# Performance work log

Measured on AMD Instinct MI355X. Metric: run time of the kernel, lower is better.

The kernel has to match this reference:

```python
import jax, jax.numpy as jnp
import numpy as np

B, S, D, H = 2, 2048, 1024, 16
DH = D // H  # key_dim = embed_dim // num_heads
NEG = 1e9    # Keras masked-softmax adder magnitude
EPS = 1e-6


def setup_inputs() -> dict:
    key = jax.random.key(0)
    ks = jax.random.split(key, 6)
    sc = 1.0 / np.sqrt(D)
    return {
        "x": jax.random.normal(ks[0], (B, S, D), jnp.float32),
        "Wq": jax.random.normal(ks[1], (D, H, DH), jnp.float32) * sc,
        "bq": jnp.zeros((H, DH), jnp.float32),
        "Wk": jax.random.normal(ks[2], (D, H, DH), jnp.float32) * sc,
        "bk": jnp.zeros((H, DH), jnp.float32),
        "Wv": jax.random.normal(ks[3], (D, H, DH), jnp.float32) * sc,
        "bv": jnp.zeros((H, DH), jnp.float32),
        "Wo": jax.random.normal(ks[4], (H, DH, D), jnp.float32) * (1.0 / np.sqrt(D)),
        "bo": jnp.zeros((D,), jnp.float32),
        "gamma": jnp.ones((D,), jnp.float32),
        "beta": jnp.zeros((D,), jnp.float32),
    }


def reference(x, Wq, bq, Wk, bk, Wv, bv, Wo, bo, gamma, beta):
    # Keras MultiHeadAttention(query=x, value=x), inference (dropouts are identity)
    q = jnp.einsum("bsd,dhk->bshk", x, Wq) + bq  # [B,S,H,DH]
    k = jnp.einsum("bsd,dhk->bshk", x, Wk) + bk
    v = jnp.einsum("bsd,dhk->bshk", x, Wv) + bv

    scores = jnp.einsum("bqhd,bkhd->bhqk", q, k) / jnp.sqrt(jnp.asarray(DH, x.dtype))
    # Source: mask = 1 - band_part(ones, -1, 0) -> ones strictly ABOVE diagonal.
    # Keras attends where mask==1 and adds (1-mask)*(-1e9) elsewhere. Faithful:
    i = jnp.arange(S)[:, None]
    j = jnp.arange(S)[None, :]
    allowed = (j > i).astype(scores.dtype)  # [S,S], strict upper triangle
    scores = scores + (allowed - 1.0) * NEG  # subtract 1e9 where not allowed
    probs = jax.nn.softmax(scores, axis=-1)

    ctx = jnp.einsum("bhqk,bkhd->bqhd", probs, v)  # [B,S,H,DH]
    attn_out = jnp.einsum("bqhd,hdo->bqo", ctx, Wo) + bo  # [B,S,D]

    # residual + LayerNorm(eps=1e-6)
    y = x + attn_out
    mu = jnp.mean(y, axis=-1, keepdims=True)
    var = jnp.mean(jnp.square(y - mu), axis=-1, keepdims=True)
    return (y - mu) * jax.lax.rsqrt(var + EPS) * gamma + beta
```

## Files before the change

### kernel.cpp

```cpp
#include <hip/hip_runtime.h>
#include <hip/hip_bf16.h>

typedef __hip_bfloat16 bf16;
typedef __attribute__((ext_vector_type(8))) short bf16x8;
typedef __attribute__((ext_vector_type(4))) float f32x4;

constexpr int Bc  = 2;
constexpr int Sc  = 2048;
constexpr int Dc  = 1024;
constexpr int Hc  = 16;
constexpr int DHc = 64;
constexpr int BS  = Bc * Sc;
constexpr int NT  = Sc / 64;

__device__ __forceinline__ float bs2f(unsigned short u) {
    union { unsigned int i; float f; } v; v.i = ((unsigned int)u) << 16; return v.f;
}
__device__ __forceinline__ short f2bs(float x) {
    bf16 h = __float2bfloat16(x);
    return *reinterpret_cast<short*>(&h);
}

typedef const __attribute__((address_space(1))) unsigned int* as1_u32p;
typedef __attribute__((address_space(3))) unsigned int* as3_u32p;
__device__ __forceinline__ void gl_lds16(const void* g, void* l) {
    __builtin_amdgcn_global_load_lds((as1_u32p)g, (as3_u32p)l, 16, 0, 0);
}

__global__ __launch_bounds__(256) void cast_x(const float* __restrict__ in,
                                              short* __restrict__ out) {
    const int i = (blockIdx.x * 256 + threadIdx.x) * 4;
    const float4 v = *(const float4*)(in + i);
    ushort4 o;
    o.x = (unsigned short)f2bs(v.x);
    o.y = (unsigned short)f2bs(v.y);
    o.z = (unsigned short)f2bs(v.z);
    o.w = (unsigned short)f2bs(v.w);
    *(ushort4*)(out + i) = o;
}

__global__ __launch_bounds__(256) void transpose_cast(
    const float* __restrict__ w0, const float* __restrict__ w1,
    const float* __restrict__ w2, const float* __restrict__ w3,
    short* __restrict__ outbase)
{
    __shared__ float T[64][65];
    const int z = blockIdx.z;
    const float* in = (z == 0) ? w0 : (z == 1) ? w1 : (z == 2) ? w2 : w3;
    short* out = outbase + (size_t)z * 1024 * 1024;
    const int k0 = blockIdx.x * 64, n0 = blockIdx.y * 64;
    const int t = threadIdx.x;
    #pragma unroll
    for (int it = 0; it < 4; ++it) {
        const int s = it * 256 + t;
        const int r = s >> 4, c = (s & 15) * 4;
        *(float4*)&T[r][c] = *(const float4*)(in + (size_t)(k0 + r) * 1024 + n0 + c);
    }
    __syncthreads();
    #pragma unroll
    for (int it = 0; it < 4; ++it) {
        const int s = it * 256 + t;
        const int rr = s >> 4, cc = (s & 15) * 4;
        ushort4 o;
        o.x = (unsigned short)f2bs(T[cc + 0][rr]);
        o.y = (unsigned short)f2bs(T[cc + 1][rr]);
        o.z = (unsigned short)f2bs(T[cc + 2][rr]);
        o.w = (unsigned short)f2bs(T[cc + 3][rr]);
        *(ushort4*)(out + (size_t)(n0 + rr) * 1024 + k0 + cc) = o;
    }
}

__global__ __launch_bounds__(256, 3) void gemm_bt(
    const short* __restrict__ A, const short* __restrict__ BTbase,
    const float* __restrict__ b0, const float* __restrict__ b1,
    const float* __restrict__ b2, short* __restrict__ Cbase,
    const float sc0)
{
    __shared__ __align__(16) short As[128 * 64];
    __shared__ __align__(16) short Bs[128 * 64];

    const int z = blockIdx.z;
    const short* BT = BTbase + (size_t)z * 1024 * 1024;
    const float* bias = (z == 0) ? b0 : (z == 1) ? b1 : b2;
    const float sc = (z == 0) ? sc0 : 1.0f;
    short* C = Cbase + (size_t)z * BS * Dc;

    const int t = threadIdx.x;
    const int lane = t & 63, w = t >> 6;
    const int quad = lane >> 4, l16 = lane & 15;
    const int wm = (w & 1) * 64, wn = (w >> 1) * 64;
    const int row0 = blockIdx.y * 128;
    const int col0 = blockIdx.x * 128;
    const int sw = l16 & 7;

    f32x4 acc[4][4] = {};

    for (int kt = 0; kt < 1024; kt += 64) {
        __syncthreads();
        #pragma unroll
        for (int i = 0; i < 4; ++i) {
            const int f = i * 256 + t;
            const int r = f >> 3;
            const int g = (f & 7) ^ (r & 7);
            short* lb = &As[(i * 256 + w * 64) * 8];
            gl_lds16(A + (size_t)(row0 + r) * 1024 + kt + g * 8, lb);
            short* lb2 = &Bs[(i * 256 + w * 64) * 8];
            gl_lds16(BT + (size_t)(col0 + r) * 1024 + kt + g * 8, lb2);
        }
        __syncthreads();
        #pragma unroll
        for (int ks = 0; ks < 2; ++ks) {
            bf16x8 av[4], bv[4];
            #pragma unroll
            for (int mt = 0; mt < 4; ++mt) {
                const int r = wm + mt * 16 + l16;
                av[mt] = *(const bf16x8*)&As[r * 64 + ((ks * 4 + quad) ^ sw) * 8];
            }
            #pragma unroll
            for (int nt = 0; nt < 4; ++nt) {
                const int r = wn + nt * 16 + l16;
                bv[nt] = *(const bf16x8*)&Bs[r * 64 + ((ks * 4 + quad) ^ sw) * 8];
            }
            #pragma unroll
            for (int mt = 0; mt < 4; ++mt)
                #pragma unroll
                for (int nt = 0; nt < 4; ++nt)
                    acc[mt][nt] = __builtin_amdgcn_mfma_f32_16x16x32_bf16(
                        av[mt], bv[nt], acc[mt][nt], 0, 0, 0);
        }
    }

    float bvv[4];
    #pragma unroll
    for (int nt = 0; nt < 4; ++nt) bvv[nt] = bias[col0 + wn + nt * 16 + l16];
    #pragma unroll
    for (int mt = 0; mt < 4; ++mt)
        #pragma unroll
        for (int reg = 0; reg < 4; ++reg) {
            const size_t row = row0 + wm + mt * 16 + quad * 4 + reg;
            #pragma unroll
            for (int nt = 0; nt < 4; ++nt) {
                const int col = col0 + wn + nt * 16 + l16;
                C[row * 1024 + col] = f2bs((acc[mt][nt][reg] + bvv[nt]) * sc);
            }
        }
}


template<bool DIAG>
__device__ __forceinline__ void qtile_step(
    const bf16x8 (&qf)[2],
    const short (&Ks)[64][72], const short (&VsT)[64][72],
    short (&Psw)[16][72],
    const int k0, const int row_base,
    const int quad, const int l16,
    float (&l)[4], f32x4 (&O)[4])
{
    bf16x8 kf[2][4];
    #pragma unroll
    for (int ks = 0; ks < 2; ++ks)
        #pragma unroll
        for (int nt = 0; nt < 4; ++nt)
            kf[ks][nt] = *(const bf16x8*)&Ks[nt * 16 + l16][ks * 32 + quad * 8];

    f32x4 S[4] = {};
    __builtin_amdgcn_s_setprio(1);
    #pragma unroll
    for (int ks = 0; ks < 2; ++ks)
        #pragma unroll
        for (int nt = 0; nt < 4; ++nt)
            S[nt] = __builtin_amdgcn_mfma_f32_16x16x32_bf16(qf[ks], kf[ks][nt], S[nt], 0, 0, 0);
    __builtin_amdgcn_s_setprio(0);

    #pragma unroll
    for (int nt = 0; nt < 4; ++nt) {
        #pragma unroll
        for (int reg = 0; reg < 4; ++reg) {
            float s = fminf(S[nt][reg], 115.4f);
            if (DIAG) {
                const int col = k0 + nt * 16 + l16;
                const int row = row_base + quad * 4 + reg;
                s = (col > row) ? s : -126.0f;
            }
            const float p = exp2f(s);
            S[nt][reg] = p;
            l[reg] += p;
        }
    }

    #pragma unroll
    for (int reg = 0; reg < 4; ++reg) {
        const __hip_bfloat162 lo = __float22bfloat162_rn(make_float2(S[0][reg], S[1][reg]));
        const __hip_bfloat162 hi = __float22bfloat162_rn(make_float2(S[2][reg], S[3][reg]));
        uint2 u;
        u.x = *reinterpret_cast<const unsigned int*>(&lo);
        u.y = *reinterpret_cast<const unsigned int*>(&hi);
        *(uint2*)&Psw[quad * 4 + reg][l16 * 4] = u;
    }

    __builtin_amdgcn_s_setprio(1);
    #pragma unroll
    for (int ks = 0; ks < 2; ++ks) {
        const bf16x8 pf = *(const bf16x8*)&Psw[l16][ks * 32 + quad * 8];
        #pragma unroll
        for (int nt = 0; nt < 4; ++nt) {
            const bf16x8 vf = *(const bf16x8*)&VsT[nt * 16 + l16][ks * 32 + quad * 8];
            O[nt] = __builtin_amdgcn_mfma_f32_16x16x32_bf16(pf, vf, O[nt], 0, 0, 0);
        }
    }
    __builtin_amdgcn_s_setprio(0);
}

__global__ __launch_bounds__(256, 4) void attn_mfma(
    const short* __restrict__ Qg, const short* __restrict__ Kg,
    const short* __restrict__ Vg, short* __restrict__ CTX)
{
    __shared__ __align__(16) short Ks [64][72];
    __shared__ __align__(16) short VsT[64][72];
    __shared__ __align__(16) short Ps[4][16][72];

    const int tid  = threadIdx.x;
    const int lane = tid & 63, w = tid >> 6;
    const int quad = lane >> 4, l16 = lane & 15;

    const int f   = blockIdx.x + 32 * blockIdx.y + 512 * blockIdx.z;
    const int xcd = f & 7;
    const int loc = f >> 3;
    const int j   = loc >> 5;
    const int lq  = loc & 31;
    const int myq = (j & 1) ? (NT - 1 - lq) : lq;
    const int bh  = xcd * 4 + j;
    const int h   = bh & 15;
    const int b   = bh >> 4;
    const size_t rb = (size_t)b * Sc;
    const int cb = h * DHc;

    const int t0 = myq;
    const int q0 = myq * 64;

    bf16x8 qf[2];
    {
        const short* qp = Qg + (rb + q0 + w * 16 + l16) * (size_t)Dc + cb + quad * 8;
        qf[0] = *(const bf16x8*)(qp);
        qf[1] = *(const bf16x8*)(qp + 32);
    }
    float l[4] = {};
    f32x4 O[4] = {};

    const int skey = tid & 63, sseg = (tid >> 6) * 8;
    const int pkey = ((skey & 15) << 2) | (skey >> 4);

    {
        const size_t g = (rb + t0 * 64 + skey) * (size_t)Dc + cb + sseg;
        const bf16x8 k0v = *(const bf16x8*)(Kg + g);
        const bf16x8 k1v = *(const bf16x8*)(Kg + g + 32);
        const bf16x8 v0v = *(const bf16x8*)(Vg + g);
        const bf16x8 v1v = *(const bf16x8*)(Vg + g + 32);
        *(bf16x8*)&Ks[skey][sseg]      = k0v;
        *(bf16x8*)&Ks[skey][sseg + 32] = k1v;
        #pragma unroll
        for (int e = 0; e < 8; ++e) {
            VsT[sseg + e][pkey]      = v0v[e];
            VsT[sseg + 32 + e][pkey] = v1v[e];
        }
    }
    __syncthreads();

    for (int t = t0; t < NT; ++t) {
        const bool havenext = (t + 1 < NT);
        bf16x8 pk0, pk1, pv0, pv1;
        if (havenext) {
            const size_t g = (rb + (t + 1) * 64 + skey) * (size_t)Dc + cb + sseg;
            pk0 = *(const bf16x8*)(Kg + g);
            pk1 = *(const bf16x8*)(Kg + g + 32);
            pv0 = *(const bf16x8*)(Vg + g);
            pv1 = *(const bf16x8*)(Vg + g + 32);
        }

        if (t == t0)
            qtile_step<true >(qf, Ks, VsT, Ps[w],
                              t * 64, q0 + w * 16, quad, l16, l, O);
        else
            qtile_step<false>(qf, Ks, VsT, Ps[w],
                              t * 64, q0 + w * 16, quad, l16, l, O);

        if (havenext) {
            __syncthreads();
            *(bf16x8*)&Ks[skey][sseg]      = pk0;
            *(bf16x8*)&Ks[skey][sseg + 32] = pk1;
            #pragma unroll
            for (int e = 0; e < 8; ++e) {
                VsT[sseg + e][pkey]      = pv0[e];
                VsT[sseg + 32 + e][pkey] = pv1[e];
            }
            __syncthreads();
        }
    }

    #pragma unroll
    for (int off = 1; off < 16; off <<= 1)
        #pragma unroll
        for (int reg = 0; reg < 4; ++reg)
            l[reg] += __shfl_xor(l[reg], off, 64);
    #pragma unroll
    for (int reg = 0; reg < 4; ++reg) l[reg] = 1.0f / l[reg];
    #pragma unroll
    for (int nt = 0; nt < 4; ++nt)
        #pragma unroll
        for (int reg = 0; reg < 4; ++reg) {
            const size_t row = rb + q0 + w * 16 + quad * 4 + reg;
            CTX[row * Dc + cb + nt * 16 + l16] = f2bs(O[nt][reg] * l[reg]);
        }
}

__global__ __launch_bounds__(256) void vmean(const short* __restrict__ V,
                                             short* __restrict__ CTX)
{
    const int h = blockIdx.x, b = blockIdx.y;
    const int t = threadIdx.x;
    const int dh = t & 63, ck = t >> 6;
    float s = 0.f;
    const short* vp = V + ((size_t)b * Sc + ck * 512) * Dc + h * DHc + dh;
    for (int j = 0; j < 512; ++j) s += bs2f(vp[(size_t)j * Dc]);
    __shared__ float red[4][64];
    red[ck][dh] = s;
    __syncthreads();
    if (ck == 0) {
        const float tot = (red[0][dh] + red[1][dh] + red[2][dh] + red[3][dh]) * (1.f / Sc);
        CTX[((size_t)b * Sc + Sc - 1) * Dc + h * DHc + dh] = f2bs(tot);
    }
}

__global__ __launch_bounds__(256, 4) void resid_ln(
    const float* __restrict__ X, const short* __restrict__ AO,
    const float* __restrict__ gamma, const float* __restrict__ beta,
    float* __restrict__ out)
{
    const int r = blockIdx.x;
    const int t = threadIdx.x;
    const size_t base = (size_t)r * Dc + t * 4;

    const float4 x4 = *(const float4*)(X + base);
    const ushort4 a4 = *(const ushort4*)(AO + base);
    float y[4];
    y[0] = x4.x + bs2f(a4.x);
    y[1] = x4.y + bs2f(a4.y);
    y[2] = x4.z + bs2f(a4.z);
    y[3] = x4.w + bs2f(a4.w);

    float s  = y[0] + y[1] + y[2] + y[3];
    float s2 = y[0]*y[0] + y[1]*y[1] + y[2]*y[2] + y[3]*y[3];
    #pragma unroll
    for (int off = 1; off < 64; off <<= 1) {
        s  += __shfl_xor(s,  off, 64);
        s2 += __shfl_xor(s2, off, 64);
    }
    __shared__ float red[8];
    const int w = t >> 6;
    if ((t & 63) == 0) { red[w] = s; red[4 + w] = s2; }
    __syncthreads();
    s  = red[0] + red[1] + red[2] + red[3];
    s2 = red[4] + red[5] + red[6] + red[7];

    const float mu   = s * (1.0f / Dc);
    const float rstd = rsqrtf(s2 * (1.0f / Dc) - mu * mu + 1e-6f);

    const float4 g4 = *(const float4*)(gamma + t * 4);
    const float4 b4 = *(const float4*)(beta  + t * 4);
    float4 o;
    o.x = (y[0] - mu) * rstd * g4.x + b4.x;
    o.y = (y[1] - mu) * rstd * g4.y + b4.y;
    o.z = (y[2] - mu) * rstd * g4.z + b4.z;
    o.w = (y[3] - mu) * rstd * g4.w + b4.w;
    *(float4*)(out + base) = o;
}

extern "C" void kernel_launch(void* const* d_in, const int* in_sizes, int n_in,
                              void* d_out, int out_size, void* d_ws, size_t ws_size,
                              hipStream_t stream)
{
    (void)in_sizes; (void)n_in; (void)out_size; (void)ws_size;
    const float* x     = (const float*)d_in[0];
    const float* Wq    = (const float*)d_in[1];
    const float* bq    = (const float*)d_in[2];
    const float* Wk    = (const float*)d_in[3];
    const float* bk    = (const float*)d_in[4];
    const float* Wv    = (const float*)d_in[5];
    const float* bv    = (const float*)d_in[6];
    const float* Wo    = (const float*)d_in[7];
    const float* bo    = (const float*)d_in[8];
    const float* gamma = (const float*)d_in[9];
    const float* beta  = (const float*)d_in[10];
    float* out = (float*)d_out;

    const size_t matN = (size_t)BS * Dc;
    const size_t wN   = (size_t)Dc * Dc;
    short* xb = (short*)d_ws;
    short* WT = xb + matN;
    short* Qb = WT + 4 * wN;
    short* Kb = Qb + matN;
    short* Vb = Kb + matN;
    short* Cx = Vb + matN;
    short* AO = Qb;

    cast_x<<<matN / 1024, 256, 0, stream>>>(x, xb);

    dim3 gt(16, 16, 4);
    transpose_cast<<<gt, 256, 0, stream>>>(Wq, Wk, Wv, Wo, WT);

    dim3 gq(Dc / 128, BS / 128, 3);
    gemm_bt<<<gq, 256, 0, stream>>>(xb, WT, bq, bk, bv, Qb, 0.18033688f);

    dim3 ga(32, 16, 2);
    attn_mfma<<<ga, 256, 0, stream>>>(Qb, Kb, Vb, Cx);

    dim3 gv(Hc, Bc);
    vmean<<<gv, 256, 0, stream>>>(Vb, Cx);

    dim3 go(Dc / 128, BS / 128, 1);
    gemm_bt<<<go, 256, 0, stream>>>(Cx, WT + 3 * wN, bo, bo, bo, AO, 1.0f);

    resid_ln<<<BS, 256, 0, stream>>>(x, AO, gamma, beta, out);
}
```

Measured before the change: 218.9 us.

## Rewrite attention kernel with 32x32x16 MFMA, XOR-swizzled LDS, double-buffered V

Replaces the per-wave 16x16x32 MFMA attention step with 32x32x16 MFMAs. The four waves form a 2x2 grid over query rows and key/dim columns, and row sums are combined across waves through shared memory. K, V and P tiles in LDS use an XOR swizzle to avoid bank conflicts. V is double-buffered so the next tile can be written without a separate sync before the stores. This is meant to cut LDS traffic and MFMA issue overhead, at the cost of more complex indexing, an extra barrier for the shared P tile, and an odd-looking V-store index expression in the prologue.

```diff
diff --git a/kernel.cpp b/kernel.cpp
--- a/kernel.cpp
+++ b/kernel.cpp
@@ -4,6 +4,7 @@
 typedef __hip_bfloat16 bf16;
 typedef __attribute__((ext_vector_type(8))) short bf16x8;
 typedef __attribute__((ext_vector_type(4))) float f32x4;
+typedef __attribute__((ext_vector_type(16))) float f32x16;
 
 constexpr int Bc  = 2;
 constexpr int Sc  = 2048;
@@ -146,82 +147,19 @@
         }
 }
 
-
-template<bool DIAG>
-__device__ __forceinline__ void qtile_step(
-    const bf16x8 (&qf)[2],
-    const short (&Ks)[64][72], const short (&VsT)[64][72],
-    short (&Psw)[16][72],
-    const int k0, const int row_base,
-    const int quad, const int l16,
-    float (&l)[4], f32x4 (&O)[4])
-{
-    bf16x8 kf[2][4];
-    #pragma unroll
-    for (int ks = 0; ks < 2; ++ks)
-        #pragma unroll
-        for (int nt = 0; nt < 4; ++nt)
-            kf[ks][nt] = *(const bf16x8*)&Ks[nt * 16 + l16][ks * 32 + quad * 8];
-
-    f32x4 S[4] = {};
-    __builtin_amdgcn_s_setprio(1);
-    #pragma unroll
-    for (int ks = 0; ks < 2; ++ks)
-        #pragma unroll
-        for (int nt = 0; nt < 4; ++nt)
-            S[nt] = __builtin_amdgcn_mfma_f32_16x16x32_bf16(qf[ks], kf[ks][nt], S[nt], 0, 0, 0);
-    __builtin_amdgcn_s_setprio(0);
-
-    #pragma unroll
-    for (int nt = 0; nt < 4; ++nt) {
-        #pragma unroll
-        for (int reg = 0; reg < 4; ++reg) {
-            float s = fminf(S[nt][reg], 115.4f);
-            if (DIAG) {
-                const int col = k0 + nt * 16 + l16;
-                const int row = row_base + quad * 4 + reg;
-                s = (col > row) ? s : -126.0f;
-            }
-            const float p = exp2f(s);
-            S[nt][reg] = p;
-            l[reg] += p;
-        }
-    }
-
-    #pragma unroll
-    for (int reg = 0; reg < 4; ++reg) {
-        const __hip_bfloat162 lo = __float22bfloat162_rn(make_float2(S[0][reg], S[1][reg]));
-        const __hip_bfloat162 hi = __float22bfloat162_rn(make_float2(S[2][reg], S[3][reg]));
-        uint2 u;
-        u.x = *reinterpret_cast<const unsigned int*>(&lo);
-        u.y = *reinterpret_cast<const unsigned int*>(&hi);
-        *(uint2*)&Psw[quad * 4 + reg][l16 * 4] = u;
-    }
-
-    __builtin_amdgcn_s_setprio(1);
-    #pragma unroll
-    for (int ks = 0; ks < 2; ++ks) {
-        const bf16x8 pf = *(const bf16x8*)&Psw[l16][ks * 32 + quad * 8];
-        #pragma unroll
-        for (int nt = 0; nt < 4; ++nt) {
-            const bf16x8 vf = *(const bf16x8*)&VsT[nt * 16 + l16][ks * 32 + quad * 8];
-            O[nt] = __builtin_amdgcn_mfma_f32_16x16x32_bf16(pf, vf, O[nt], 0, 0, 0);
-        }
-    }
-    __builtin_amdgcn_s_setprio(0);
-}
-
 __global__ __launch_bounds__(256, 4) void attn_mfma(
     const short* __restrict__ Qg, const short* __restrict__ Kg,
     const short* __restrict__ Vg, short* __restrict__ CTX)
 {
-    __shared__ __align__(16) short Ks [64][72];
-    __shared__ __align__(16) short VsT[64][72];
-    __shared__ __align__(16) short Ps[4][16][72];
+    __shared__ __align__(16) short Ks[64 * 72];
+    __shared__ __align__(16) short Vs[2][64 * 72];
+    __shared__ __align__(16) short Ps[2][32 * 72];
+    __shared__ float lred[2][2][32];
 
     const int tid  = threadIdx.x;
     const int lane = tid & 63, w = tid >> 6;
-    const int quad = lane >> 4, l16 = lane & 15;
+    const int n32  = lane & 31, hh = lane >> 5;
+    const int g    = w & 1, r = w >> 1;
 
     const int f   = blockIdx.x + 32 * blockIdx.y + 512 * blockIdx.z;
     const int xcd = f & 7;
@@ -238,79 +176,146 @@
     const int t0 = myq;
     const int q0 = myq * 64;
 
-    bf16x8 qf[2];
+    bf16x8 qf[4];
     {
-        const short* qp = Qg + (rb + q0 + w * 16 + l16) * (size_t)Dc + cb + quad * 8;
-        qf[0] = *(const bf16x8*)(qp);
-        qf[1] = *(const bf16x8*)(qp + 32);
-    }
-    float l[4] = {};
-    f32x4 O[4] = {};
-
-    const int skey = tid & 63, sseg = (tid >> 6) * 8;
-    const int pkey = ((skey & 15) << 2) | (skey >> 4);
+        const short* qp = Qg + (rb + q0 + r * 32 + n32) * (size_t)Dc + cb + hh * 8;
+        #pragma unroll
+        for (int k = 0; k < 4; ++k) qf[k] = *(const bf16x8*)(qp + k * 16);
+    }
+
+    float l[16] = {};
+    f32x16 O = {};
+
+    const int skey = tid & 63, u1 = tid >> 6, sseg = u1 * 8;
+    const int sk7 = skey & 7;
 
     {
-        const size_t g = (rb + t0 * 64 + skey) * (size_t)Dc + cb + sseg;
-        const bf16x8 k0v = *(const bf16x8*)(Kg + g);
-        const bf16x8 k1v = *(const bf16x8*)(Kg + g + 32);
-        const bf16x8 v0v = *(const bf16x8*)(Vg + g);
-        const bf16x8 v1v = *(const bf16x8*)(Vg + g + 32);
-        *(bf16x8*)&Ks[skey][sseg]      = k0v;
-        *(bf16x8*)&Ks[skey][sseg + 32] = k1v;
+        const size_t ga = (rb + t0 * 64 + skey) * (size_t)Dc + cb + sseg;
+        const bf16x8 k0v = *(const bf16x8*)(Kg + ga);
+        const bf16x8 k1v = *(const bf16x8*)(Kg + ga + 32);
+        const bf16x8 v0v = *(const bf16x8*)(Vg + ga);
+        const bf16x8 v1v = *(const bf16x8*)(Vg + ga + 32);
+        short* Krow = &Ks[skey * 72];
+        *(bf16x8*)&Krow[(u1 ^ sk7) * 8]       = k0v;
+        *(bf16x8*)&Krow[((u1 + 4) ^ sk7) * 8] = k1v;
         #pragma unroll
         for (int e = 0; e < 8; ++e) {
-            VsT[sseg + e][pkey]      = v0v[e];
-            VsT[sseg + 32 + e][pkey] = v1v[e];
+            const int d0 = sseg + e, d1 = d0 + 32;
+            Vs[0][d0 * 72 + ((((skey >> 3) ^ e) << 3) | sk7 ? 0 : 0) + (((skey >> 3) ^ (d0 & 7)) << 3) + (skey & 7) - ((((skey >> 3) ^ e) << 3) | sk7 ? 0 : 0)] = v0v[e];
+            Vs[0][d1 * 72 + (((skey >> 3) ^ (d1 & 7)) << 3) + (skey & 7)] = v1v[e];
         }
     }
     __syncthreads();
+
+    int cur = 0;
+    const int key = g * 32 + n32;
+    const int k7  = key & 7;
+    const int n7  = n32 & 7;
 
     for (int t = t0; t < NT; ++t) {
         const bool havenext = (t + 1 < NT);
         bf16x8 pk0, pk1, pv0, pv1;
         if (havenext) {
-            const size_t g = (rb + (t + 1) * 64 + skey) * (size_t)Dc + cb + sseg;
-            pk0 = *(const bf16x8*)(Kg + g);
-            pk1 = *(const bf16x8*)(Kg + g + 32);
-            pv0 = *(const bf16x8*)(Vg + g);
-            pv1 = *(const bf16x8*)(Vg + g + 32);
-        }
-
-        if (t == t0)
-            qtile_step<true >(qf, Ks, VsT, Ps[w],
-                              t * 64, q0 + w * 16, quad, l16, l, O);
-        else
-            qtile_step<false>(qf, Ks, VsT, Ps[w],
-                              t * 64, q0 + w * 16, quad, l16, l, O);
+            const size_t ga = (rb + (t + 1) * 64 + skey) * (size_t)Dc + cb + sseg;
+            pk0 = *(const bf16x8*)(Kg + ga);
+            pk1 = *(const bf16x8*)(Kg + ga + 32);
+            pv0 = *(const bf16x8*)(Vg + ga);
+            pv1 = *(const bf16x8*)(Vg + ga + 32);
+        }
+
+        f32x16 S = {};
+        {
+            const short* KsRow = &Ks[key * 72];
+            bf16x8 kf[4];
+            #pragma unroll
+            for (int k = 0; k < 4; ++k)
+                kf[k] = *(const bf16x8*)&KsRow[((k * 2 + hh) ^ k7) * 8];
+            __builtin_amdgcn_s_setprio(1);
+            #pragma unroll
+            for (int k = 0; k < 4; ++k)
+                S = __builtin_amdgcn_mfma_f32_32x32x16_bf16(qf[k], kf[k], S, 0, 0, 0);
+            __builtin_amdgcn_s_setprio(0);
+        }
+
+        short* Pr = &Ps[r][0];
+        if (t == t0) {
+            #pragma unroll
+            for (int reg = 0; reg < 16; ++reg) {
+                const int qloc = (reg & 3) + 8 * (reg >> 2) + 4 * hh;
+                const int col = t * 64 + key;
+                const int row = q0 + r * 32 + qloc;
+                float s = fminf(S[reg], 115.4f);
+                s = (col > row) ? s : -126.0f;
+                const float p = exp2f(s);
+                l[reg] += p;
+                const int unit = (g * 4 + (n32 >> 3)) ^ (qloc & 7);
+                Pr[qloc * 72 + unit * 8 + n7] = f2bs(p);
+            }
+        } else {
+            #pragma unroll
+            for (int reg = 0; reg < 16; ++reg) {
+                const int qloc = (reg & 3) + 8 * (reg >> 2) + 4 * hh;
+                const float p = exp2f(fminf(S[reg], 115.4f));
+                l[reg] += p;
+                const int unit = (g * 4 + (n32 >> 3)) ^ (qloc & 7);
+                Pr[qloc * 72 + unit * 8 + n7] = f2bs(p);
+            }
+        }
+
+        __syncthreads();
+
+        {
+            const int d = g * 32 + n32;
+            const short* Vrow = &Vs[cur][d * 72];
+            const short* Prow = &Ps[r][n32 * 72];
+            bf16x8 pf[4], vf[4];
+            #pragma unroll
+            for (int k = 0; k < 4; ++k) {
+                const int off = ((k * 2 + hh) ^ n7) * 8;
+                pf[k] = *(const bf16x8*)&Prow[off];
+                vf[k] = *(const bf16x8*)&Vrow[off];
+            }
+            __builtin_amdgcn_s_setprio(1);
+            #pragma unroll
+            for (int k = 0; k < 4; ++k)
+                O = __builtin_amdgcn_mfma_f32_32x32x16_bf16(pf[k], vf[k], O, 0, 0, 0);
+            __builtin_amdgcn_s_setprio(0);
+        }
 
         if (havenext) {
+            short* Krow = &Ks[skey * 72];
+            *(bf16x8*)&Krow[(u1 ^ sk7) * 8]       = pk0;
+            *(bf16x8*)&Krow[((u1 + 4) ^ sk7) * 8] = pk1;
+            short* Vn = &Vs[cur ^ 1][0];
+            #pragma unroll
+            for (int e = 0; e < 8; ++e) {
+                const int d0 = sseg + e, d1 = d0 + 32;
+                Vn[d0 * 72 + (((skey >> 3) ^ (d0 & 7)) << 3) + (skey & 7)] = pv0[e];
+                Vn[d1 * 72 + (((skey >> 3) ^ (d1 & 7)) << 3) + (skey & 7)] = pv1[e];
+            }
             __syncthreads();
-            *(bf16x8*)&Ks[skey][sseg]      = pk0;
-            *(bf16x8*)&Ks[skey][sseg + 32] = pk1;
-            #pragma unroll
-            for (int e = 0; e < 8; ++e) {
-                VsT[sseg + e][pkey]      = pv0[e];
-                VsT[sseg + 32 + e][pkey] = pv1[e];
-            }
-            __syncthreads();
-        }
-    }
-
-    #pragma unroll
-    for (int off = 1; off < 16; off <<= 1)
-        #pragma unroll
-        for (int reg = 0; reg < 4; ++reg)
+            cur ^= 1;
+        }
+    }
+
+    #pragma unroll
+    for (int off = 1; off < 32; off <<= 1)
+        #pragma unroll
+        for (int reg = 0; reg < 16; ++reg)
             l[reg] += __shfl_xor(l[reg], off, 64);
-    #pragma unroll
-    for (int reg = 0; reg < 4; ++reg) l[reg] = 1.0f / l[reg];
-    #pragma unroll
-    for (int nt = 0; nt < 4; ++nt)
-        #pragma unroll
-        for (int reg = 0; reg < 4; ++reg) {
-            const size_t row = rb + q0 + w * 16 + quad * 4 + reg;
-            CTX[row * Dc + cb + nt * 16 + l16] = f2bs(O[nt][reg] * l[reg]);
-        }
+    if (n32 == 0) {
+        #pragma unroll
+        for (int reg = 0; reg < 16; ++reg)
+            lred[g][r][(reg & 3) + 8 * (reg >> 2) + 4 * hh] = l[reg];
+    }
+    __syncthreads();
+    #pragma unroll
+    for (int reg = 0; reg < 16; ++reg) {
+        const int qloc = (reg & 3) + 8 * (reg >> 2) + 4 * hh;
+        const float inv = 1.0f / (lred[0][r][qloc] + lred[1][r][qloc]);
+        const size_t row = rb + q0 + r * 32 + qloc;
+        CTX[row * Dc + cb + g * 32 + n32] = f2bs(O[reg] * inv);
+    }
 }
 
 __global__ __launch_bounds__(256) void vmean(const short* __restrict__ V,
```

Result: slower. 333.1 us (+52.1%).
